# Optimization experiments

Measured on AMD Instinct MI355X. Metric: run time of the kernel, lower is better.

Reference implementation:

```python
import jax, jax.numpy as jnp
import numpy as np

N_NODES = 50000
N_EDGES = 800000
NODE_DIM = 256
HIDDEN_DIM = 256
LN_EPS = 1e-5


def setup_inputs() -> dict:
    key = jax.random.key(0)
    ks = jax.random.split(key, 8)
    d, h = NODE_DIM, HIDDEN_DIM
    return {
        "node_features": jax.random.normal(ks[0], (N_NODES, d), jnp.float32),
        "src": jax.random.randint(ks[1], (N_EDGES,), 0, N_NODES, jnp.int32),
        "dst": jax.random.randint(ks[2], (N_EDGES,), 0, N_NODES, jnp.int32),
        "edge_weight": jax.random.uniform(ks[3], (N_EDGES,), jnp.float32),
        "W1": jax.random.normal(ks[4], (d, h), jnp.float32) / np.sqrt(d),
        "b1": jnp.zeros((h,), jnp.float32),
        "g1": jnp.ones((h,), jnp.float32),
        "be1": jnp.zeros((h,), jnp.float32),
        "W2": jax.random.normal(ks[5], (h, h), jnp.float32) / np.sqrt(h),
        "b2": jnp.zeros((h,), jnp.float32),
        "g2": jnp.ones((h,), jnp.float32),
        "be2": jnp.zeros((h,), jnp.float32),
        "Wp": jax.random.normal(ks[6], (h, d), jnp.float32) / np.sqrt(h),
        "bp": jnp.zeros((d,), jnp.float32),
    }


def _spmm(src, dst, w, x, n):
    # sparse adj @ x : agg[i] = sum_{edges e with dst=i} w_e * x[src_e]
    return jax.ops.segment_sum(w[:, None] * x[src], dst, num_segments=n)


def _layer_norm(x, g, b):
    mu = jnp.mean(x, -1, keepdims=True)
    var = jnp.mean(jnp.square(x - mu), -1, keepdims=True)
    return (x - mu) * jax.lax.rsqrt(var + LN_EPS) * g + b


def reference(node_features, src, dst, edge_weight, W1, b1, g1, be1, W2, b2, g2, be2, Wp, bp):
    n = node_features.shape[0]
    x = node_features
    for (W, b, g, be) in ((W1, b1, g1, be1), (W2, b2, g2, be2)):
        agg = _spmm(src, dst, edge_weight, x, n)
        h = (x + agg) @ W + b
        x = jax.nn.gelu(_layer_norm(h, g, be), approximate=False)
        # Dropout(0.1) is identity in eval mode
    return x @ Wp + bp
```

## Files before the change

kernel.cpp:

```cpp
#include <hip/hip_runtime.h>
#include <hip/hip_bf16.h>
#include <math.h>

#define N_NODES 50000
#define N_EDGES 800000
#define DIM 256
#define MPAD 50176
#define LN_EPS 1e-5f
#define SCAN_BLOCKS 196
#define LDB 264

typedef short bf16x8 __attribute__((ext_vector_type(8)));
typedef float f32x4 __attribute__((ext_vector_type(4)));
typedef unsigned short u16;
typedef u16 u16x8 __attribute__((ext_vector_type(8)));

__device__ __forceinline__ u16 f2bf(float f) {
    union { float f; unsigned u; } v; v.f = f;
    unsigned r = (v.u + 0x7FFFu + ((v.u >> 16) & 1u)) >> 16;
    return (u16)r;
}
__device__ __forceinline__ float bf2f(u16 h) {
    union { unsigned u; float f; } v; v.u = ((unsigned)h) << 16;
    return v.f;
}
__device__ __forceinline__ float gelu_f(float x) {
    float z = x * (1.595769122f + 0.0713548162726f * x * x);
    return x * (1.0f / (1.0f + __expf(-z)));
}

__global__ void count_kernel(const int* __restrict__ dst, int* __restrict__ counts) {
    int e = blockIdx.x * 256 + threadIdx.x;
    if (e < N_EDGES) atomicAdd(&counts[dst[e]], 1);
}

__global__ void scan1_kernel(const int* __restrict__ counts, int* __restrict__ offsets,
                             int* __restrict__ bsum) {
    __shared__ int sh[256];
    int t = threadIdx.x;
    int idx = blockIdx.x * 256 + t;
    int v = (idx < N_NODES) ? counts[idx] : 0;
    sh[t] = v;
    __syncthreads();
#pragma unroll
    for (int off = 1; off < 256; off <<= 1) {
        int u = (t >= off) ? sh[t - off] : 0;
        __syncthreads();
        sh[t] += u;
        __syncthreads();
    }
    if (idx < N_NODES) offsets[idx] = sh[t] - v;
    if (t == 255) bsum[blockIdx.x] = sh[255];
}

__global__ void scan2_kernel(const int* __restrict__ bsum, int* __restrict__ bbase) {
    __shared__ int sh[256];
    int t = threadIdx.x;
    int v = (t < SCAN_BLOCKS) ? bsum[t] : 0;
    sh[t] = v;
    __syncthreads();
#pragma unroll
    for (int off = 1; off < 256; off <<= 1) {
        int u = (t >= off) ? sh[t - off] : 0;
        __syncthreads();
        sh[t] += u;
        __syncthreads();
    }
    if (t < SCAN_BLOCKS) bbase[t] = sh[t] - v;
}

__global__ void scan3_kernel(int* __restrict__ offsets, const int* __restrict__ bbase,
                             int* __restrict__ cursor) {
    int idx = blockIdx.x * 256 + threadIdx.x;
    if (idx < N_NODES) {
        int o = offsets[idx] + bbase[blockIdx.x];
        offsets[idx] = o;
        cursor[idx] = o;
    }
    if (idx == 0) offsets[N_NODES] = N_EDGES;
}

__global__ void scatter_kernel(const int* __restrict__ src, const int* __restrict__ dst,
                               const float* __restrict__ w, int* __restrict__ cursor,
                               int* __restrict__ sperm, float* __restrict__ wperm) {
    int e = blockIdx.x * 256 + threadIdx.x;
    if (e < N_EDGES) {
        int d = dst[e];
        int p = atomicAdd(&cursor[d], 1);
        sperm[p] = src[e];
        wperm[p] = w[e];
    }
}

__global__ void conv_kernel(const float* __restrict__ in, u16* __restrict__ out) {
    int i = blockIdx.x * 256 + threadIdx.x;
    float4 v = ((const float4*)in)[i];
    ushort4 o;
    o.x = f2bf(v.x); o.y = f2bf(v.y); o.z = f2bf(v.z); o.w = f2bf(v.w);
    ((ushort4*)out)[i] = o;
}

__global__ void convw_kernel(const float* __restrict__ W1, const float* __restrict__ W2,
                             const float* __restrict__ Wp, u16* __restrict__ WT) {
    int idx = blockIdx.x * 256 + threadIdx.x;
    int m = idx >> 16;
    int r = idx & 65535;
    int n = r >> 8, k = r & 255;
    const float* W = (m == 0) ? W1 : (m == 1) ? W2 : Wp;
    WT[idx] = f2bf(W[k * 256 + n]);
}

__global__ __launch_bounds__(256) void spmm_kernel(
        const u16* __restrict__ x, const int* __restrict__ offs,
        const int* __restrict__ sperm, const float* __restrict__ wperm,
        u16* __restrict__ y) {
    __shared__ u16 tile[16 * 256];
    int tid = threadIdx.x;
    int wave = tid >> 6;
    int lane = tid & 63;
    int node0 = blockIdx.x * 16 + wave * 4;

    const ushort4* xv = (const ushort4*)x;
#pragma unroll 1
    for (int i = 0; i < 4; ++i) {
        int node = node0 + i;
        ushort4 v = xv[(size_t)node * 64 + lane];
        float a0 = bf2f(v.x), a1 = bf2f(v.y), a2 = bf2f(v.z), a3 = bf2f(v.w);
        float b0 = 0, b1 = 0, b2 = 0, b3 = 0;
        float c0 = 0, c1 = 0, c2 = 0, c3 = 0;
        float d0 = 0, d1 = 0, d2 = 0, d3 = 0;

        int p = offs[node];
        int p1 = offs[node + 1];
        for (; p + 4 <= p1; p += 4) {
            int s0 = sperm[p], s1 = sperm[p + 1], s2 = sperm[p + 2], s3 = sperm[p + 3];
            float w0 = wperm[p], w1 = wperm[p + 1], w2 = wperm[p + 2], w3 = wperm[p + 3];
            ushort4 v0 = xv[(size_t)s0 * 64 + lane];
            ushort4 v1 = xv[(size_t)s1 * 64 + lane];
            ushort4 v2 = xv[(size_t)s2 * 64 + lane];
            ushort4 v3 = xv[(size_t)s3 * 64 + lane];
            a0 += w0 * bf2f(v0.x); a1 += w0 * bf2f(v0.y); a2 += w0 * bf2f(v0.z); a3 += w0 * bf2f(v0.w);
            b0 += w1 * bf2f(v1.x); b1 += w1 * bf2f(v1.y); b2 += w1 * bf2f(v1.z); b3 += w1 * bf2f(v1.w);
            c0 += w2 * bf2f(v2.x); c1 += w2 * bf2f(v2.y); c2 += w2 * bf2f(v2.z); c3 += w2 * bf2f(v2.w);
            d0 += w3 * bf2f(v3.x); d1 += w3 * bf2f(v3.y); d2 += w3 * bf2f(v3.z); d3 += w3 * bf2f(v3.w);
        }
        for (; p < p1; ++p) {
            int s = sperm[p];
            float w = wperm[p];
            ushort4 vv = xv[(size_t)s * 64 + lane];
            a0 += w * bf2f(vv.x); a1 += w * bf2f(vv.y); a2 += w * bf2f(vv.z); a3 += w * bf2f(vv.w);
        }
        a0 += b0 + c0 + d0; a1 += b1 + c1 + d1;
        a2 += b2 + c2 + d2; a3 += b3 + c3 + d3;
        ushort4 o;
        o.x = f2bf(a0); o.y = f2bf(a1); o.z = f2bf(a2); o.w = f2bf(a3);
        ((ushort4*)&tile[(wave * 4 + i) * 256])[lane] = o;
    }
    __syncthreads();
    u16* outb = y + (size_t)blockIdx.x * 4096;
#pragma unroll
    for (int h = 0; h < 2; ++h) {
        int gI = tid + h * 256;
        int r = gI & 15;
        int k0 = (gI >> 6) * 32 + ((gI >> 4) & 3) * 8;
        u16x8 v = *(const u16x8*)&tile[r * 256 + k0];
        *(u16x8*)(outb + (size_t)gI * 8) = v;
    }
}

template <int MODE, int OUT_TILED>
__global__ __launch_bounds__(256, 1) void gemm_kernel(
        const u16* __restrict__ A, const u16* __restrict__ BT,
        const float* __restrict__ bias, const float* __restrict__ g,
        const float* __restrict__ be, u16* __restrict__ xb_out,
        float* __restrict__ f_out) {
    __shared__ u16 b_lds[256 * LDB];
    int tid = threadIdx.x;
    int wave = tid >> 6, lane = tid & 63;
    int quad = lane >> 4, l15 = lane & 15;

#pragma unroll
    for (int i = 0; i < 32; ++i) {
        int c = i * 256 + tid;
        u16x8 v = *(const u16x8*)(BT + (size_t)c * 8);
        *(u16x8*)&b_lds[(c >> 5) * LDB + (c & 31) * 8] = v;
    }

    int tbase = blockIdx.x * 16 + wave * 4;
    const u16* ga0 = A + (size_t)(tbase + 0) * 4096 + lane * 8;
    const u16* ga1 = A + (size_t)(tbase + 1) * 4096 + lane * 8;
    const u16* ga2 = A + (size_t)(tbase + 2) * 4096 + lane * 8;
    const u16* ga3 = A + (size_t)(tbase + 3) * 4096 + lane * 8;
    bf16x8 p0 = *(const bf16x8*)ga0;
    bf16x8 p1 = *(const bf16x8*)ga1;
    bf16x8 p2 = *(const bf16x8*)ga2;
    bf16x8 p3 = *(const bf16x8*)ga3;

    f32x4 acc[4][16];
#pragma unroll
    for (int rf = 0; rf < 4; ++rf)
#pragma unroll
        for (int t = 0; t < 16; ++t) acc[rf][t] = {0.f, 0.f, 0.f, 0.f};

    __syncthreads();

#pragma unroll
    for (int kb = 0; kb < 8; ++kb) {
        bf16x8 a0 = p0, a1 = p1, a2 = p2, a3 = p3;
        if (kb < 7) {
            p0 = *(const bf16x8*)(ga0 + (kb + 1) * 512);
            p1 = *(const bf16x8*)(ga1 + (kb + 1) * 512);
            p2 = *(const bf16x8*)(ga2 + (kb + 1) * 512);
            p3 = *(const bf16x8*)(ga3 + (kb + 1) * 512);
        }
        const u16* bl = &b_lds[l15 * LDB + kb * 32 + quad * 8];
#pragma unroll
        for (int t = 0; t < 16; ++t) {
            bf16x8 bf = *(const bf16x8*)(bl + t * 16 * LDB);
            acc[0][t] = __builtin_amdgcn_mfma_f32_16x16x32_bf16(a0, bf, acc[0][t], 0, 0, 0);
            acc[1][t] = __builtin_amdgcn_mfma_f32_16x16x32_bf16(a1, bf, acc[1][t], 0, 0, 0);
            acc[2][t] = __builtin_amdgcn_mfma_f32_16x16x32_bf16(a2, bf, acc[2][t], 0, 0, 0);
            acc[3][t] = __builtin_amdgcn_mfma_f32_16x16x32_bf16(a3, bf, acc[3][t], 0, 0, 0);
        }
    }

    int rowblk = blockIdx.x * 256 + wave * 64;
#pragma unroll
    for (int rf = 0; rf < 4; ++rf) {
        int rbase = rowblk + rf * 16 + quad * 4;
        if (MODE == 0) {
#pragma unroll
            for (int t = 0; t < 16; ++t) {
                float bv = bias[t * 16 + l15];
#pragma unroll
                for (int i = 0; i < 4; ++i) acc[rf][t][i] += bv;
            }
#pragma unroll
            for (int i = 0; i < 4; ++i) {
                float s = 0.f, q = 0.f;
#pragma unroll
                for (int t = 0; t < 16; ++t) { float v = acc[rf][t][i]; s += v; q += v * v; }
                for (int off = 1; off < 16; off <<= 1) {
                    s += __shfl_xor(s, off);
                    q += __shfl_xor(q, off);
                }
                float mu = s * (1.0f / 256.0f);
                float var = q * (1.0f / 256.0f) - mu * mu;
                float rs = rsqrtf(var + LN_EPS);
                int row = rbase + i;
#pragma unroll
                for (int t = 0; t < 16; ++t) {
                    int c = t * 16 + l15;
                    float v = (acc[rf][t][i] - mu) * rs * g[c] + be[c];
                    u16 ob = f2bf(gelu_f(v));
                    if (OUT_TILED) {
                        size_t o = (size_t)(row >> 4) * 4096 + (c >> 5) * 512 +
                                   ((c >> 3) & 3) * 128 + (row & 15) * 8 + (c & 7);
                        xb_out[o] = ob;
                    } else {
                        xb_out[(size_t)row * 256 + c] = ob;
                    }
                }
            }
        } else {
#pragma unroll
            for (int i = 0; i < 4; ++i) {
                int row = rbase + i;
                if (row < N_NODES) {
#pragma unroll
                    for (int t = 0; t < 16; ++t) {
                        int c = t * 16 + l15;
                        f_out[(size_t)row * 256 + c] = acc[rf][t][i] + bias[c];
                    }
                }
            }
        }
    }
}

extern "C" void kernel_launch(void* const* d_in, const int* in_sizes, int n_in,
                              void* d_out, int out_size, void* d_ws, size_t ws_size,
                              hipStream_t stream) {
    const float* nodef = (const float*)d_in[0];
    const int*   src   = (const int*)d_in[1];
    const int*   dst   = (const int*)d_in[2];
    const float* ew    = (const float*)d_in[3];
    const float* W1 = (const float*)d_in[4];
    const float* b1 = (const float*)d_in[5];
    const float* g1 = (const float*)d_in[6];
    const float* be1 = (const float*)d_in[7];
    const float* W2 = (const float*)d_in[8];
    const float* b2 = (const float*)d_in[9];
    const float* g2 = (const float*)d_in[10];
    const float* be2 = (const float*)d_in[11];
    const float* Wp = (const float*)d_in[12];
    const float* bp = (const float*)d_in[13];
    float* out = (float*)d_out;

    char* ws = (char*)d_ws;
    size_t off = 0;
    auto alloc = [&](size_t bytes) -> void* {
        void* p = ws + off;
        off += (bytes + 255) & ~(size_t)255;
        return p;
    };
    u16*   ybuf    = (u16*)alloc((size_t)MPAD * 256 * 2);
    u16*   xbuf    = (u16*)alloc((size_t)MPAD * 256 * 2);
    u16*   WT      = (u16*)alloc((size_t)3 * 65536 * 2);
    int*   counts  = (int*)alloc((size_t)N_NODES * 4);
    int*   offsets = (int*)alloc((size_t)(N_NODES + 1) * 4);
    int*   cursor  = (int*)alloc((size_t)N_NODES * 4);
    int*   sperm   = (int*)alloc((size_t)N_EDGES * 4);
    float* wperm   = (float*)alloc((size_t)N_EDGES * 4);
    int*   bsum    = (int*)alloc((size_t)SCAN_BLOCKS * 4);
    int*   bbase   = (int*)alloc((size_t)SCAN_BLOCKS * 4);

    hipMemsetAsync(counts, 0, (size_t)N_NODES * 4, stream);
    count_kernel<<<(N_EDGES + 255) / 256, 256, 0, stream>>>(dst, counts);
    scan1_kernel<<<SCAN_BLOCKS, 256, 0, stream>>>(counts, offsets, bsum);
    scan2_kernel<<<1, 256, 0, stream>>>(bsum, bbase);
    scan3_kernel<<<SCAN_BLOCKS, 256, 0, stream>>>(offsets, bbase, cursor);
    scatter_kernel<<<(N_EDGES + 255) / 256, 256, 0, stream>>>(src, dst, ew, cursor, sperm, wperm);
    conv_kernel<<<N_NODES * 64 / 256, 256, 0, stream>>>(nodef, xbuf);
    convw_kernel<<<768, 256, 0, stream>>>(W1, W2, Wp, WT);

    const int GB = MPAD / 256;
    const int SB = N_NODES / 16;
    spmm_kernel<<<SB, 256, 0, stream>>>(xbuf, offsets, sperm, wperm, ybuf);
    gemm_kernel<0, 0><<<GB, 256, 0, stream>>>(ybuf, WT, b1, g1, be1, xbuf, nullptr);
    spmm_kernel<<<SB, 256, 0, stream>>>(xbuf, offsets, sperm, wperm, ybuf);
    gemm_kernel<0, 1><<<GB, 256, 0, stream>>>(ybuf, WT + 65536, b2, g2, be2, ybuf, nullptr);
    gemm_kernel<1, 0><<<GB, 256, 0, stream>>>(ybuf, WT + 2 * 65536, bp, nullptr, nullptr, nullptr, out);
}
```

Before: 447.7 us.

## Switch GEMM to 32x32x16 MFMA with matching 32-row tiled A and B layouts

Replaces the 16x16x32 bf16 MFMA tiles in the fused GEMM+LayerNorm+GELU kernel with 32x32x16 MFMAs. The tiled activation layout written by the SpMM and by the layer-1 epilogue, and the LDS layout of B, are changed to match. SpMM now handles 32 nodes per block and guards padded rows. The aim is to cut LDS reads of B per FLOP and raise MFMA efficiency, at the cost of a more complex epilogue, a 32-lane reduction and more scattered output writes.

```diff
diff --git a/kernel.cpp b/kernel.cpp
--- a/kernel.cpp
+++ b/kernel.cpp
@@ -8,10 +8,9 @@
 #define MPAD 50176
 #define LN_EPS 1e-5f
 #define SCAN_BLOCKS 196
-#define LDB 264
 
 typedef short bf16x8 __attribute__((ext_vector_type(8)));
-typedef float f32x4 __attribute__((ext_vector_type(4)));
+typedef float f32x16 __attribute__((ext_vector_type(16)));
 typedef unsigned short u16;
 typedef u16 u16x8 __attribute__((ext_vector_type(8)));
 
@@ -114,57 +113,60 @@
         const u16* __restrict__ x, const int* __restrict__ offs,
         const int* __restrict__ sperm, const float* __restrict__ wperm,
         u16* __restrict__ y) {
-    __shared__ u16 tile[16 * 256];
+    __shared__ u16 tile[32 * 264];
     int tid = threadIdx.x;
     int wave = tid >> 6;
     int lane = tid & 63;
-    int node0 = blockIdx.x * 16 + wave * 4;
+    int node0 = blockIdx.x * 32 + wave * 8;
 
     const ushort4* xv = (const ushort4*)x;
 #pragma unroll 1
-    for (int i = 0; i < 4; ++i) {
+    for (int i = 0; i < 8; ++i) {
         int node = node0 + i;
-        ushort4 v = xv[(size_t)node * 64 + lane];
-        float a0 = bf2f(v.x), a1 = bf2f(v.y), a2 = bf2f(v.z), a3 = bf2f(v.w);
+        float a0 = 0, a1 = 0, a2 = 0, a3 = 0;
         float b0 = 0, b1 = 0, b2 = 0, b3 = 0;
         float c0 = 0, c1 = 0, c2 = 0, c3 = 0;
         float d0 = 0, d1 = 0, d2 = 0, d3 = 0;
-
-        int p = offs[node];
-        int p1 = offs[node + 1];
-        for (; p + 4 <= p1; p += 4) {
-            int s0 = sperm[p], s1 = sperm[p + 1], s2 = sperm[p + 2], s3 = sperm[p + 3];
-            float w0 = wperm[p], w1 = wperm[p + 1], w2 = wperm[p + 2], w3 = wperm[p + 3];
-            ushort4 v0 = xv[(size_t)s0 * 64 + lane];
-            ushort4 v1 = xv[(size_t)s1 * 64 + lane];
-            ushort4 v2 = xv[(size_t)s2 * 64 + lane];
-            ushort4 v3 = xv[(size_t)s3 * 64 + lane];
-            a0 += w0 * bf2f(v0.x); a1 += w0 * bf2f(v0.y); a2 += w0 * bf2f(v0.z); a3 += w0 * bf2f(v0.w);
-            b0 += w1 * bf2f(v1.x); b1 += w1 * bf2f(v1.y); b2 += w1 * bf2f(v1.z); b3 += w1 * bf2f(v1.w);
-            c0 += w2 * bf2f(v2.x); c1 += w2 * bf2f(v2.y); c2 += w2 * bf2f(v2.z); c3 += w2 * bf2f(v2.w);
-            d0 += w3 * bf2f(v3.x); d1 += w3 * bf2f(v3.y); d2 += w3 * bf2f(v3.z); d3 += w3 * bf2f(v3.w);
+        if (node < N_NODES) {
+            ushort4 v = xv[(size_t)node * 64 + lane];
+            a0 = bf2f(v.x); a1 = bf2f(v.y); a2 = bf2f(v.z); a3 = bf2f(v.w);
+            int p = offs[node];
+            int p1 = offs[node + 1];
+            for (; p + 4 <= p1; p += 4) {
+                int s0 = sperm[p], s1 = sperm[p + 1], s2 = sperm[p + 2], s3 = sperm[p + 3];
+                float w0 = wperm[p], w1 = wperm[p + 1], w2 = wperm[p + 2], w3 = wperm[p + 3];
+                ushort4 v0 = xv[(size_t)s0 * 64 + lane];
+                ushort4 v1 = xv[(size_t)s1 * 64 + lane];
+                ushort4 v2 = xv[(size_t)s2 * 64 + lane];
+                ushort4 v3 = xv[(size_t)s3 * 64 + lane];
+                a0 += w0 * bf2f(v0.x); a1 += w0 * bf2f(v0.y); a2 += w0 * bf2f(v0.z); a3 += w0 * bf2f(v0.w);
+                b0 += w1 * bf2f(v1.x); b1 += w1 * bf2f(v1.y); b2 += w1 * bf2f(v1.z); b3 += w1 * bf2f(v1.w);
+                c0 += w2 * bf2f(v2.x); c1 += w2 * bf2f(v2.y); c2 += w2 * bf2f(v2.z); c3 += w2 * bf2f(v2.w);
+                d0 += w3 * bf2f(v3.x); d1 += w3 * bf2f(v3.y); d2 += w3 * bf2f(v3.z); d3 += w3 * bf2f(v3.w);
+            }
+            for (; p < p1; ++p) {
+                int s = sperm[p];
+                float w = wperm[p];
+                ushort4 vv = xv[(size_t)s * 64 + lane];
+                a0 += w * bf2f(vv.x); a1 += w * bf2f(vv.y); a2 += w * bf2f(vv.z); a3 += w * bf2f(vv.w);
+            }
+            a0 += b0 + c0 + d0; a1 += b1 + c1 + d1;
+            a2 += b2 + c2 + d2; a3 += b3 + c3 + d3;
         }
-        for (; p < p1; ++p) {
-            int s = sperm[p];
-            float w = wperm[p];
-            ushort4 vv = xv[(size_t)s * 64 + lane];
-            a0 += w * bf2f(vv.x); a1 += w * bf2f(vv.y); a2 += w * bf2f(vv.z); a3 += w * bf2f(vv.w);
-        }
-        a0 += b0 + c0 + d0; a1 += b1 + c1 + d1;
-        a2 += b2 + c2 + d2; a3 += b3 + c3 + d3;
         ushort4 o;
         o.x = f2bf(a0); o.y = f2bf(a1); o.z = f2bf(a2); o.w = f2bf(a3);
-        ((ushort4*)&tile[(wave * 4 + i) * 256])[lane] = o;
+        ((ushort4*)&tile[(wave * 8 + i) * 264])[lane] = o;
     }
     __syncthreads();
-    u16* outb = y + (size_t)blockIdx.x * 4096;
-#pragma unroll
-    for (int h = 0; h < 2; ++h) {
-        int gI = tid + h * 256;
-        int r = gI & 15;
-        int k0 = (gI >> 6) * 32 + ((gI >> 4) & 3) * 8;
-        u16x8 v = *(const u16x8*)&tile[r * 256 + k0];
-        *(u16x8*)(outb + (size_t)gI * 8) = v;
+    u16* outb = y + (size_t)blockIdx.x * 8192;
+#pragma unroll
+    for (int hh = 0; hh < 4; ++hh) {
+        int gi = tid + hh * 256;
+        int kb = gi >> 6;
+        int rem = gi & 63;
+        int hf = rem >> 5, m = rem & 31;
+        u16x8 v = *(const u16x8*)&tile[m * 264 + kb * 16 + hf * 8];
+        *(u16x8*)(outb + (size_t)gi * 8) = v;
     }
 }
 
@@ -174,88 +176,92 @@
         const float* __restrict__ bias, const float* __restrict__ g,
         const float* __restrict__ be, u16* __restrict__ xb_out,
         float* __restrict__ f_out) {
-    __shared__ u16 b_lds[256 * LDB];
+    __shared__ u16 b_lds[128 * 520];
     int tid = threadIdx.x;
     int wave = tid >> 6, lane = tid & 63;
-    int quad = lane >> 4, l15 = lane & 15;
-
-#pragma unroll
+    int l31 = lane & 31, half = lane >> 5;
+
+#pragma unroll 8
     for (int i = 0; i < 32; ++i) {
-        int c = i * 256 + tid;
-        u16x8 v = *(const u16x8*)(BT + (size_t)c * 8);
-        *(u16x8*)&b_lds[(c >> 5) * LDB + (c & 31) * 8] = v;
-    }
-
-    int tbase = blockIdx.x * 16 + wave * 4;
-    const u16* ga0 = A + (size_t)(tbase + 0) * 4096 + lane * 8;
-    const u16* ga1 = A + (size_t)(tbase + 1) * 4096 + lane * 8;
-    const u16* ga2 = A + (size_t)(tbase + 2) * 4096 + lane * 8;
-    const u16* ga3 = A + (size_t)(tbase + 3) * 4096 + lane * 8;
+        int s = i * 256 + tid;
+        u16x8 v = *(const u16x8*)(BT + (size_t)s * 8);
+        int n = s >> 5, kc = s & 31;
+        int t = n >> 5, n32 = n & 31, kb = kc >> 1, hf = kc & 1;
+        *(u16x8*)&b_lds[(t * 16 + kb) * 520 + hf * 256 + n32 * 8] = v;
+    }
+
+    int tile0 = blockIdx.x * 8 + wave * 2;
+    const u16* ga0 = A + (size_t)tile0 * 8192 + lane * 8;
+    const u16* ga1 = ga0 + 8192;
     bf16x8 p0 = *(const bf16x8*)ga0;
     bf16x8 p1 = *(const bf16x8*)ga1;
-    bf16x8 p2 = *(const bf16x8*)ga2;
-    bf16x8 p3 = *(const bf16x8*)ga3;
-
-    f32x4 acc[4][16];
-#pragma unroll
-    for (int rf = 0; rf < 4; ++rf)
-#pragma unroll
-        for (int t = 0; t < 16; ++t) acc[rf][t] = {0.f, 0.f, 0.f, 0.f};
+
+    f32x16 acc[2][8];
+#pragma unroll
+    for (int rf = 0; rf < 2; ++rf)
+#pragma unroll
+        for (int t = 0; t < 8; ++t)
+#pragma unroll
+            for (int r = 0; r < 16; ++r) acc[rf][t][r] = 0.f;
 
     __syncthreads();
 
 #pragma unroll
-    for (int kb = 0; kb < 8; ++kb) {
-        bf16x8 a0 = p0, a1 = p1, a2 = p2, a3 = p3;
-        if (kb < 7) {
+    for (int kb = 0; kb < 16; ++kb) {
+        bf16x8 a0 = p0, a1 = p1;
+        if (kb < 15) {
             p0 = *(const bf16x8*)(ga0 + (kb + 1) * 512);
             p1 = *(const bf16x8*)(ga1 + (kb + 1) * 512);
-            p2 = *(const bf16x8*)(ga2 + (kb + 1) * 512);
-            p3 = *(const bf16x8*)(ga3 + (kb + 1) * 512);
         }
-        const u16* bl = &b_lds[l15 * LDB + kb * 32 + quad * 8];
-#pragma unroll
-        for (int t = 0; t < 16; ++t) {
-            bf16x8 bf = *(const bf16x8*)(bl + t * 16 * LDB);
-            acc[0][t] = __builtin_amdgcn_mfma_f32_16x16x32_bf16(a0, bf, acc[0][t], 0, 0, 0);
-            acc[1][t] = __builtin_amdgcn_mfma_f32_16x16x32_bf16(a1, bf, acc[1][t], 0, 0, 0);
-            acc[2][t] = __builtin_amdgcn_mfma_f32_16x16x32_bf16(a2, bf, acc[2][t], 0, 0, 0);
-            acc[3][t] = __builtin_amdgcn_mfma_f32_16x16x32_bf16(a3, bf, acc[3][t], 0, 0, 0);
+        const u16* bl = &b_lds[kb * 520 + lane * 8];
+#pragma unroll
+        for (int t = 0; t < 8; ++t) {
+            bf16x8 bf = *(const bf16x8*)(bl + t * 16 * 520);
+            acc[0][t] = __builtin_amdgcn_mfma_f32_32x32x16_bf16(a0, bf, acc[0][t], 0, 0, 0);
+            acc[1][t] = __builtin_amdgcn_mfma_f32_32x32x16_bf16(a1, bf, acc[1][t], 0, 0, 0);
         }
     }
 
-    int rowblk = blockIdx.x * 256 + wave * 64;
-#pragma unroll
-    for (int rf = 0; rf < 4; ++rf) {
-        int rbase = rowblk + rf * 16 + quad * 4;
+    float bv[8];
+#pragma unroll
+    for (int t = 0; t < 8; ++t) bv[t] = bias[t * 32 + l31];
+
+#pragma unroll
+    for (int rf = 0; rf < 2; ++rf) {
+        int tile = tile0 + rf;
         if (MODE == 0) {
-#pragma unroll
-            for (int t = 0; t < 16; ++t) {
-                float bv = bias[t * 16 + l15];
-#pragma unroll
-                for (int i = 0; i < 4; ++i) acc[rf][t][i] += bv;
-            }
-#pragma unroll
-            for (int i = 0; i < 4; ++i) {
+            float gv[8], bev[8];
+#pragma unroll
+            for (int t = 0; t < 8; ++t) {
+                int c = t * 32 + l31;
+                gv[t] = g[c]; bev[t] = be[c];
+            }
+#pragma unroll
+            for (int r = 0; r < 16; ++r) {
                 float s = 0.f, q = 0.f;
 #pragma unroll
-                for (int t = 0; t < 16; ++t) { float v = acc[rf][t][i]; s += v; q += v * v; }
-                for (int off = 1; off < 16; off <<= 1) {
+                for (int t = 0; t < 8; ++t) {
+                    float v = acc[rf][t][r] + bv[t];
+                    acc[rf][t][r] = v;
+                    s += v; q += v * v;
+                }
+                for (int off = 1; off < 32; off <<= 1) {
                     s += __shfl_xor(s, off);
                     q += __shfl_xor(q, off);
                 }
                 float mu = s * (1.0f / 256.0f);
                 float var = q * (1.0f / 256.0f) - mu * mu;
                 float rs = rsqrtf(var + LN_EPS);
-                int row = rbase + i;
-#pragma unroll
-                for (int t = 0; t < 16; ++t) {
-                    int c = t * 16 + l15;
-                    float v = (acc[rf][t][i] - mu) * rs * g[c] + be[c];
+                int m = (r & 3) + 8 * (r >> 2) + 4 * half;
+                int row = tile * 32 + m;
+#pragma unroll
+                for (int t = 0; t < 8; ++t) {
+                    int c = t * 32 + l31;
+                    float v = (acc[rf][t][r] - mu) * rs * gv[t] + bev[t];
                     u16 ob = f2bf(gelu_f(v));
                     if (OUT_TILED) {
-                        size_t o = (size_t)(row >> 4) * 4096 + (c >> 5) * 512 +
-                                   ((c >> 3) & 3) * 128 + (row & 15) * 8 + (c & 7);
+                        size_t o = (size_t)tile * 8192 +
+                                   ((size_t)(c >> 4) * 64 + ((c >> 3) & 1) * 32 + m) * 8 + (c & 7);
                         xb_out[o] = ob;
                     } else {
                         xb_out[(size_t)row * 256 + c] = ob;
@@ -264,13 +270,14 @@
             }
         } else {
 #pragma unroll
-            for (int i = 0; i < 4; ++i) {
-                int row = rbase + i;
+            for (int r = 0; r < 16; ++r) {
+                int m = (r & 3) + 8 * (r >> 2) + 4 * half;
+                int row = tile * 32 + m;
                 if (row < N_NODES) {
 #pragma unroll
-                    for (int t = 0; t < 16; ++t) {
-                        int c = t * 16 + l15;
-                        f_out[(size_t)row * 256 + c] = acc[rf][t][i] + bias[c];
+                    for (int t = 0; t < 8; ++t) {
+                        int c = t * 32 + l31;
+                        f_out[(size_t)row * 256 + c] = acc[rf][t][r] + bv[t];
                     }
                 }
             }
@@ -325,7 +332,7 @@
     convw_kernel<<<768, 256, 0, stream>>>(W1, W2, Wp, WT);
 
     const int GB = MPAD / 256;
-    const int SB = N_NODES / 16;
+    const int SB = MPAD / 32;
     spmm_kernel<<<SB, 256, 0, stream>>>(xbuf, offsets, sperm, wperm, ybuf);
     gemm_kernel<0, 0><<<GB, 256, 0, stream>>>(ybuf, WT, b1, g1, be1, xbuf, nullptr);
     spmm_kernel<<<SB, 256, 0, stream>>>(xbuf, offsets, sperm, wperm, ybuf);
```

After: 447.5 us. About the same (-0.1%).
